# Optimization experiments

Hardware: AMD Instinct MI355X
Metric: run time of the kernel (lower is better)

## Reference

```python
import jax, jax.numpy as jnp
import numpy as np

N_NODES = 100000
N_EDGES = 1600000
DIM_IN, DIM_H, DIM_OUT = 128, 128, 64


def setup_inputs() -> dict:
    key = jax.random.key(0)
    ks = jax.random.split(key, 8)
    s = 0.05
    return {
        "x": jax.random.normal(ks[0], (N_NODES, DIM_IN), jnp.float32),
        "edge_index": jax.random.randint(ks[1], (2, N_EDGES), 0, N_NODES, jnp.int64),
        "W_l1": jax.random.normal(ks[2], (DIM_IN, DIM_H), jnp.float32) * s,
        "W_r1": jax.random.normal(ks[3], (DIM_IN, DIM_H), jnp.float32) * s,
        "b1": jax.random.normal(ks[4], (DIM_H,), jnp.float32) * s,
        "W_l2": jax.random.normal(ks[5], (DIM_H, DIM_OUT), jnp.float32) * s,
        "W_r2": jax.random.normal(ks[6], (DIM_H, DIM_OUT), jnp.float32) * s,
        "b2": jax.random.normal(ks[7], (DIM_OUT,), jnp.float32) * s,
    }


def _sage_conv(h, src, dst, n_nodes, W_l, W_r, b):
    # mean-aggregate neighbor features: gather x[src], scatter-sum to dst, divide by in-degree
    msg = h[src]                                              # [E, d]
    agg = jax.ops.segment_sum(msg, dst, num_segments=n_nodes)  # [N, d]
    deg = jax.ops.segment_sum(jnp.ones((src.shape[0],), h.dtype), dst, num_segments=n_nodes)
    mean = agg / jnp.maximum(deg, 1.0)[:, None]
    # out = lin_l(mean) + lin_r(x) ; bias lives on lin_l (PyG SAGEConv default)
    return mean @ W_l + h @ W_r + b


def reference(x, edge_index, W_l1, W_r1, b1, W_l2, W_r2, b2):
    src, dst = edge_index[0], edge_index[1]
    n = x.shape[0]
    h = jax.nn.relu(_sage_conv(x, src, dst, n, W_l1, W_r1, b1))
    # dropout(p=0.5) is identity in eval mode
    return _sage_conv(h, src, dst, n, W_l2, W_r2, b2)
```

## Files before the change

### kernel.cpp

```cpp
#include <hip/hip_runtime.h>

#define NN 100000
#define NE 1600000

typedef __attribute__((ext_vector_type(8))) short bf16x8;
typedef __attribute__((ext_vector_type(4))) float f32x4;

__device__ __forceinline__ float bf2f(unsigned short b) {
    union { unsigned int u; float f; } v;
    v.u = ((unsigned int)b) << 16;
    return v.f;
}
__device__ __forceinline__ unsigned short f2bf(float f) {
    union { float f; unsigned int u; } v; v.f = f;
    unsigned int u = v.u;
    return (unsigned short)((u + 0x7FFFu + ((u >> 16) & 1u)) >> 16);
}

__global__ void detect_kernel(const int* __restrict__ e, int* __restrict__ flag) {
    int t = blockIdx.x * blockDim.x + threadIdx.x;
    if (t < 4096 && e[2 * t + 1] != 0) atomicOr(flag, 1);
}

__device__ __forceinline__ int esrc(const int* e, int mode, int i) {
    return mode ? e[i] : e[2 * i];
}
__device__ __forceinline__ int edst(const int* e, int mode, int i) {
    return mode ? e[NE + i] : e[2 * (NE + i)];
}

__global__ __launch_bounds__(256) void wcvt_kernel(
    const float* __restrict__ W_l1, const float* __restrict__ W_r1,
    const float* __restrict__ W_l2, const float* __restrict__ W_r2,
    unsigned short* __restrict__ wt) {
    int b = blockIdx.x;
    const float* src; unsigned short* dst; int NO, tk, tn;
    if (b < 4)       { src = W_l1; dst = wt;         NO = 128; tk = b >> 1; tn = b & 1; }
    else if (b < 8)  { b -= 4; src = W_r1; dst = wt + 16384; NO = 128; tk = b >> 1; tn = b & 1; }
    else if (b < 10) { b -= 8; src = W_l2; dst = wt + 32768; NO = 64; tk = b; tn = 0; }
    else             { b -= 10; src = W_r2; dst = wt + 40960; NO = 64; tk = b; tn = 0; }
    __shared__ unsigned short lt[64][72];
    const int r0 = tk * 64, c0 = tn * 64;
    const int lr = threadIdx.x >> 6;
    const int lc = threadIdx.x & 63;
#pragma unroll
    for (int i = 0; i < 16; i++) {
        int r = lr * 16 + i;
        lt[lc][r] = f2bf(src[(size_t)(r0 + r) * NO + c0 + lc]);
    }
    __syncthreads();
#pragma unroll
    for (int i = 0; i < 16; i++) {
        int n = lr * 16 + i;
        dst[(size_t)(c0 + n) * 128 + r0 + lc] = lt[n][lc];
    }
}

#define NRANGE 4
#define RSZ 25000
#define NCHUNK 64
#define EPC (NE / NCHUNK)
#define GS 100352

__global__ __launch_bounds__(1024) void histA_kernel(
    const int* __restrict__ e, const int* __restrict__ flag, int* __restrict__ G) {
    __shared__ int lh[RSZ];
    const int bid = blockIdx.x;
    const int r = bid & (NRANGE - 1);
    const int c = bid >> 2;
    const int lo = r * RSZ;
    for (int idx = threadIdx.x; idx < RSZ; idx += 1024) lh[idx] = 0;
    __syncthreads();
    const int mode = *flag;
    const int base = c * EPC;
    for (int i = base + threadIdx.x; i < base + EPC; i += 1024) {
        int dl = edst(e, mode, i) - lo;
        if ((unsigned)dl < (unsigned)RSZ) atomicAdd(&lh[dl], 1);
    }
    __syncthreads();
    for (int idx = threadIdx.x; idx < RSZ; idx += 1024)
        G[(size_t)c * GS + lo + idx] = lh[idx];
}

__global__ __launch_bounds__(1024) void scatterC_kernel(
    const int* __restrict__ e, const int* __restrict__ flag,
    const int* __restrict__ S, const int* __restrict__ G, int* __restrict__ csr) {
    __shared__ int sOff[RSZ];
    const int bid = blockIdx.x;
    const int r = bid & (NRANGE - 1);
    const int c = bid >> 2;
    const int lo = r * RSZ;
    for (int idx = threadIdx.x; idx < RSZ; idx += 1024)
        sOff[idx] = S[lo + idx] + G[(size_t)c * GS + lo + idx];
    __syncthreads();
    const int mode = *flag;
    const int base = c * EPC;
    for (int i = base + threadIdx.x; i < base + EPC; i += 1024) {
        int dl = edst(e, mode, i) - lo;
        if ((unsigned)dl < (unsigned)RSZ) {
            int s = esrc(e, mode, i);
            csr[atomicAdd(&sOff[dl], 1)] = s;
        }
    }
}

#define PREF_B 391
#define CVT_G 6250

__global__ __launch_bounds__(256) void prefix_cvt_kernel(
    int* __restrict__ G, int* __restrict__ S,
    const float* __restrict__ xin, unsigned short* __restrict__ xb) {
    if (blockIdx.x < PREF_B) {
        int d = blockIdx.x * 256 + threadIdx.x;
        if (d >= NN) return;
        int run = 0;
#pragma unroll 8
        for (int c = 0; c < NCHUNK; c++) {
            size_t idx = (size_t)c * GS + d;
            int t = G[idx];
            G[idx] = run;
            run += t;
        }
        S[d] = run;
    } else {
        long long i = ((long long)(blockIdx.x - PREF_B) * 256 + threadIdx.x) * 8;
        float4 a = *(const float4*)(xin + i);
        float4 b = *(const float4*)(xin + i + 4);
        bf16x8 rv;
        rv[0] = (short)f2bf(a.x); rv[1] = (short)f2bf(a.y);
        rv[2] = (short)f2bf(a.z); rv[3] = (short)f2bf(a.w);
        rv[4] = (short)f2bf(b.x); rv[5] = (short)f2bf(b.y);
        rv[6] = (short)f2bf(b.z); rv[7] = (short)f2bf(b.w);
        *(bf16x8*)(xb + i) = rv;
    }
}

#define SCAN_G 392

__global__ __launch_bounds__(256) void blocksum_kernel(const int* __restrict__ S,
                                                       int* __restrict__ part) {
    int i = blockIdx.x * 256 + threadIdx.x;
    int v = (i < NN) ? S[i] : 0;
#pragma unroll
    for (int off = 32; off; off >>= 1) v += __shfl_down(v, off, 64);
    __shared__ int wsum[4];
    if ((threadIdx.x & 63) == 0) wsum[threadIdx.x >> 6] = v;
    __syncthreads();
    if (threadIdx.x == 0)
        part[blockIdx.x] = wsum[0] + wsum[1] + wsum[2] + wsum[3];
}

__global__ __launch_bounds__(512) void partscan_kernel(int* __restrict__ part) {
    __shared__ int lds[512];
    const int t = threadIdx.x;
    int v = (t < SCAN_G) ? part[t] : 0;
    lds[t] = v;
    __syncthreads();
    for (int off = 1; off < 512; off <<= 1) {
        int u = (t >= off) ? lds[t - off] : 0;
        __syncthreads();
        lds[t] += u;
        __syncthreads();
    }
    if (t < SCAN_G) part[t] = lds[t] - v;
}

__global__ __launch_bounds__(256) void scanfin_kernel(int* __restrict__ S,
                                                      const int* __restrict__ part) {
    __shared__ int lds[256];
    const int t = threadIdx.x;
    const int i = blockIdx.x * 256 + t;
    int v = (i < NN) ? S[i] : 0;
    lds[t] = v;
    __syncthreads();
    for (int off = 1; off < 256; off <<= 1) {
        int u = (t >= off) ? lds[t - off] : 0;
        __syncthreads();
        lds[t] += u;
        __syncthreads();
    }
    if (i < NN) S[i] = lds[t] - v + part[blockIdx.x];
}

__global__ __launch_bounds__(256) void gather_mean128(
    const unsigned short* __restrict__ feat, const int* __restrict__ csr,
    const int* __restrict__ S, unsigned short* __restrict__ out) {
    const int tid = threadIdx.x;
    const int node = blockIdx.x * 16 + (tid >> 4);
    const int c = tid & 15;
    if (node >= NN) return;
    const int begin = S[node];
    const int end = (node == NN - 1) ? NE : S[node + 1];
    float acc0[8] = {0.f, 0.f, 0.f, 0.f, 0.f, 0.f, 0.f, 0.f};
    float acc1[8] = {0.f, 0.f, 0.f, 0.f, 0.f, 0.f, 0.f, 0.f};
    int j = begin;
    for (; j + 4 <= end; j += 4) {
        int s0 = csr[j], s1 = csr[j + 1], s2 = csr[j + 2], s3 = csr[j + 3];
        bf16x8 v0 = *(const bf16x8*)(feat + (size_t)s0 * 128 + 8 * c);
        bf16x8 v1 = *(const bf16x8*)(feat + (size_t)s1 * 128 + 8 * c);
        bf16x8 v2 = *(const bf16x8*)(feat + (size_t)s2 * 128 + 8 * c);
        bf16x8 v3 = *(const bf16x8*)(feat + (size_t)s3 * 128 + 8 * c);
#pragma unroll
        for (int q = 0; q < 8; q++) {
            acc0[q] += bf2f((unsigned short)v0[q]) + bf2f((unsigned short)v2[q]);
            acc1[q] += bf2f((unsigned short)v1[q]) + bf2f((unsigned short)v3[q]);
        }
    }
    for (; j < end; j++) {
        int s = csr[j];
        bf16x8 v = *(const bf16x8*)(feat + (size_t)s * 128 + 8 * c);
#pragma unroll
        for (int q = 0; q < 8; q++) acc0[q] += bf2f((unsigned short)v[q]);
    }
    const float inv = 1.0f / fmaxf((float)(end - begin), 1.0f);
    bf16x8 r;
#pragma unroll
    for (int q = 0; q < 8; q++) r[q] = (short)f2bf((acc0[q] + acc1[q]) * inv);
    *(bf16x8*)(out + (size_t)node * 128 + 8 * c) = r;
}

__global__ __launch_bounds__(256) void gemm1_kernel(
    const unsigned short* __restrict__ A,
    const unsigned short* __restrict__ X,
    const unsigned short* __restrict__ WaT,
    const unsigned short* __restrict__ WbT,
    const float* __restrict__ b1,
    unsigned short* __restrict__ H, int N) {
    const int tid = threadIdx.x;
    const int lane = tid & 63;
    const int wv = tid >> 6;
    const int r16 = lane & 15;
    const int kg = lane >> 4;
    const long long rowbase = (long long)blockIdx.x * 128 + wv * 32;

    bf16x8 xf[2][4], af[2][4];
    const bf16x8 zz = {0, 0, 0, 0, 0, 0, 0, 0};
#pragma unroll
    for (int rt = 0; rt < 2; rt++) {
        long long row = rowbase + rt * 16 + r16;
        bool ok = row < N;
#pragma unroll
        for (int ks = 0; ks < 4; ks++) {
            xf[rt][ks] = ok ? *(const bf16x8*)(X + row * 128 + ks * 32 + kg * 8) : zz;
            af[rt][ks] = ok ? *(const bf16x8*)(A + row * 128 + ks * 32 + kg * 8) : zz;
        }
    }

    f32x4 acc[2][8];
#pragma unroll
    for (int t = 0; t < 8; t++) {
        float bv = b1[t * 16 + r16];
#pragma unroll
        for (int rt = 0; rt < 2; rt++) acc[rt][t] = (f32x4){bv, bv, bv, bv};
    }

#pragma unroll
    for (int t = 0; t < 8; t++) {
        const unsigned short* wb = WbT + (size_t)(t * 16 + r16) * 128 + kg * 8;
        const unsigned short* wa = WaT + (size_t)(t * 16 + r16) * 128 + kg * 8;
        bf16x8 bb[4], ba[4];
#pragma unroll
        for (int ks = 0; ks < 4; ks++) {
            bb[ks] = *(const bf16x8*)(wb + ks * 32);
            ba[ks] = *(const bf16x8*)(wa + ks * 32);
        }
#pragma unroll
        for (int rt = 0; rt < 2; rt++) {
#pragma unroll
            for (int ks = 0; ks < 4; ks++) {
                acc[rt][t] = __builtin_amdgcn_mfma_f32_16x16x32_bf16(
                    xf[rt][ks], bb[ks], acc[rt][t], 0, 0, 0);
                acc[rt][t] = __builtin_amdgcn_mfma_f32_16x16x32_bf16(
                    af[rt][ks], ba[ks], acc[rt][t], 0, 0, 0);
            }
        }
    }

#pragma unroll
    for (int rt = 0; rt < 2; rt++)
#pragma unroll
        for (int r = 0; r < 4; r++) {
            long long row = rowbase + rt * 16 + kg * 4 + r;
            if (row < N)
#pragma unroll
                for (int t = 0; t < 8; t++)
                    H[row * 128 + t * 16 + r16] = f2bf(fmaxf(acc[rt][t][r], 0.f));
        }
}

__global__ __launch_bounds__(256) void gemm23_kernel(
    const unsigned short* __restrict__ Hb,
    const unsigned short* __restrict__ WlT,
    const unsigned short* __restrict__ WrT,
    const float* __restrict__ b2,
    unsigned short* __restrict__ T2, unsigned short* __restrict__ P3, int N) {
    const int tid = threadIdx.x;
    const int lane = tid & 63;
    const int wv = tid >> 6;
    const int r16 = lane & 15;
    const int kg = lane >> 4;
    const long long rowbase = (long long)blockIdx.x * 128 + wv * 32;

    bf16x8 hf[2][4];
    const bf16x8 zz = {0, 0, 0, 0, 0, 0, 0, 0};
#pragma unroll
    for (int rt = 0; rt < 2; rt++) {
        long long row = rowbase + rt * 16 + r16;
        bool ok = row < N;
#pragma unroll
        for (int ks = 0; ks < 4; ks++)
            hf[rt][ks] = ok ? *(const bf16x8*)(Hb + row * 128 + ks * 32 + kg * 8) : zz;
    }

    f32x4 ot[2][4], op[2][4];
#pragma unroll
    for (int t = 0; t < 4; t++) {
        float bv = b2[t * 16 + r16];
#pragma unroll
        for (int rt = 0; rt < 2; rt++) {
            ot[rt][t] = (f32x4){0.f, 0.f, 0.f, 0.f};
            op[rt][t] = (f32x4){bv, bv, bv, bv};
        }
    }

#pragma unroll
    for (int t = 0; t < 4; t++) {
        const unsigned short* wl = WlT + (size_t)(t * 16 + r16) * 128 + kg * 8;
        const unsigned short* wr = WrT + (size_t)(t * 16 + r16) * 128 + kg * 8;
        bf16x8 bl[4], br[4];
#pragma unroll
        for (int ks = 0; ks < 4; ks++) {
            bl[ks] = *(const bf16x8*)(wl + ks * 32);
            br[ks] = *(const bf16x8*)(wr + ks * 32);
        }
#pragma unroll
        for (int rt = 0; rt < 2; rt++) {
#pragma unroll
            for (int ks = 0; ks < 4; ks++) {
                ot[rt][t] = __builtin_amdgcn_mfma_f32_16x16x32_bf16(
                    hf[rt][ks], bl[ks], ot[rt][t], 0, 0, 0);
                op[rt][t] = __builtin_amdgcn_mfma_f32_16x16x32_bf16(
                    hf[rt][ks], br[ks], op[rt][t], 0, 0, 0);
            }
        }
    }

#pragma unroll
    for (int rt = 0; rt < 2; rt++)
#pragma unroll
        for (int r = 0; r < 4; r++) {
            long long row = rowbase + rt * 16 + kg * 4 + r;
            if (row < N)
#pragma unroll
                for (int t = 0; t < 4; t++) {
                    T2[row * 64 + t * 16 + r16] = f2bf(ot[rt][t][r]);
                    P3[row * 64 + t * 16 + r16] = f2bf(op[rt][t][r]);
                }
        }
}

__global__ __launch_bounds__(256) void gather2_fused(
    const unsigned short* __restrict__ t2, const unsigned short* __restrict__ p3,
    const int* __restrict__ csr, const int* __restrict__ S, float* __restrict__ out) {
    const int tid = threadIdx.x;
    const int node = blockIdx.x * 32 + (tid >> 3);
    const int c = tid & 7;
    if (node >= NN) return;
    const int begin = S[node];
    const int end = (node == NN - 1) ? NE : S[node + 1];
    float acc0[8] = {0.f, 0.f, 0.f, 0.f, 0.f, 0.f, 0.f, 0.f};
    float acc1[8] = {0.f, 0.f, 0.f, 0.f, 0.f, 0.f, 0.f, 0.f};
    int j = begin;
    for (; j + 4 <= end; j += 4) {
        int s0 = csr[j], s1 = csr[j + 1], s2 = csr[j + 2], s3 = csr[j + 3];
        bf16x8 v0 = *(const bf16x8*)(t2 + (size_t)s0 * 64 + 8 * c);
        bf16x8 v1 = *(const bf16x8*)(t2 + (size_t)s1 * 64 + 8 * c);
        bf16x8 v2 = *(const bf16x8*)(t2 + (size_t)s2 * 64 + 8 * c);
        bf16x8 v3 = *(const bf16x8*)(t2 + (size_t)s3 * 64 + 8 * c);
#pragma unroll
        for (int q = 0; q < 8; q++) {
            acc0[q] += bf2f((unsigned short)v0[q]) + bf2f((unsigned short)v2[q]);
            acc1[q] += bf2f((unsigned short)v1[q]) + bf2f((unsigned short)v3[q]);
        }
    }
    for (; j < end; j++) {
        int s = csr[j];
        bf16x8 v = *(const bf16x8*)(t2 + (size_t)s * 64 + 8 * c);
#pragma unroll
        for (int q = 0; q < 8; q++) acc0[q] += bf2f((unsigned short)v[q]);
    }
    const float inv = 1.0f / fmaxf((float)(end - begin), 1.0f);
    bf16x8 pv = *(const bf16x8*)(p3 + (size_t)node * 64 + 8 * c);
    f32x4 r0, r1;
#pragma unroll
    for (int q = 0; q < 4; q++) {
        r0[q] = (acc0[q] + acc1[q]) * inv + bf2f((unsigned short)pv[q]);
        r1[q] = (acc0[4 + q] + acc1[4 + q]) * inv + bf2f((unsigned short)pv[4 + q]);
    }
    *(f32x4*)(out + (size_t)node * 64 + 8 * c) = r0;
    *(f32x4*)(out + (size_t)node * 64 + 8 * c + 4) = r1;
}

extern "C" void kernel_launch(void* const* d_in, const int* in_sizes, int n_in,
                              void* d_out, int out_size, void* d_ws, size_t ws_size,
                              hipStream_t stream) {
    const float* x    = (const float*)d_in[0];
    const int*   e32  = (const int*)d_in[1];
    const float* W_l1 = (const float*)d_in[2];
    const float* W_r1 = (const float*)d_in[3];
    const float* b1   = (const float*)d_in[4];
    const float* W_l2 = (const float*)d_in[5];
    const float* W_r2 = (const float*)d_in[6];
    const float* b2   = (const float*)d_in[7];
    float* out = (float*)d_out;

    int* wsI = (int*)d_ws;
    int* flag = wsI;
    int* S    = wsI + 1024;
    int* part = wsI + 101376;
    int* csr  = wsI + 101888;
    unsigned short* xb = (unsigned short*)(wsI + 1701888);
    unsigned short* t2b = (unsigned short*)(wsI + 1701888);
    unsigned short* p3b = (unsigned short*)(wsI + 4901888);
    int* G = wsI + 8101888;
    unsigned short* mean1b = (unsigned short*)(wsI + 8101888);
    unsigned short* hb     = (unsigned short*)(wsI + 14524416);
    unsigned short* wt     = (unsigned short*)(wsI + 20924416);

    hipMemsetAsync(d_ws, 0, 4096, stream);

    detect_kernel<<<16, 256, 0, stream>>>(e32, flag);
    wcvt_kernel<<<12, 256, 0, stream>>>(W_l1, W_r1, W_l2, W_r2, wt);
    histA_kernel<<<NRANGE * NCHUNK, 1024, 0, stream>>>(e32, flag, G);
    prefix_cvt_kernel<<<PREF_B + CVT_G, 256, 0, stream>>>(G, S, x, xb);
    blocksum_kernel<<<SCAN_G, 256, 0, stream>>>(S, part);
    partscan_kernel<<<1, 512, 0, stream>>>(part);
    scanfin_kernel<<<SCAN_G, 256, 0, stream>>>(S, part);
    scatterC_kernel<<<NRANGE * NCHUNK, 1024, 0, stream>>>(e32, flag, S, G, csr);

    gather_mean128<<<6250, 256, 0, stream>>>(xb, csr, S, mean1b);

    gemm1_kernel<<<782, 256, 0, stream>>>(mean1b, xb, wt, wt + 16384, b1, hb, NN);

    gemm23_kernel<<<782, 256, 0, stream>>>(hb, wt + 32768, wt + 40960, b2,
                                           t2b, p3b, NN);

    gather2_fused<<<3125, 256, 0, stream>>>(t2b, p3b, csr, S, out);
}
```

Before: 237.3 us.

## Store features column-blocked and split gathers into per-XCD column groups

The node feature buffers (x in bf16, mean1, h, t2) move from row-major to a column-group-major layout of 16-element groups. The gather kernels are split so each block handles one column group, chosen by blockIdx & 7 so it lines up with XCD round-robin scheduling. Each group's slice is then smaller and more likely to stay in one XCD's L2 during the random neighbor reads. Weight conversion to bf16 is folded into the GEMM kernels through LDS, which removes a launch but redoes the conversion in every block. The gathers also spread edges across lanes with shuffle reductions and use nontemporal loads and stores.

```diff
diff --git a/kernel.cpp b/kernel.cpp
--- a/kernel.cpp
+++ b/kernel.cpp
@@ -2,6 +2,7 @@
 
 #define NN 100000
 #define NE 1600000
+#define NN16 ((size_t)NN * 16)
 
 typedef __attribute__((ext_vector_type(8))) short bf16x8;
 typedef __attribute__((ext_vector_type(4))) float f32x4;
@@ -27,33 +28,6 @@
 }
 __device__ __forceinline__ int edst(const int* e, int mode, int i) {
     return mode ? e[NE + i] : e[2 * (NE + i)];
-}
-
-__global__ __launch_bounds__(256) void wcvt_kernel(
-    const float* __restrict__ W_l1, const float* __restrict__ W_r1,
-    const float* __restrict__ W_l2, const float* __restrict__ W_r2,
-    unsigned short* __restrict__ wt) {
-    int b = blockIdx.x;
-    const float* src; unsigned short* dst; int NO, tk, tn;
-    if (b < 4)       { src = W_l1; dst = wt;         NO = 128; tk = b >> 1; tn = b & 1; }
-    else if (b < 8)  { b -= 4; src = W_r1; dst = wt + 16384; NO = 128; tk = b >> 1; tn = b & 1; }
-    else if (b < 10) { b -= 8; src = W_l2; dst = wt + 32768; NO = 64; tk = b; tn = 0; }
-    else             { b -= 10; src = W_r2; dst = wt + 40960; NO = 64; tk = b; tn = 0; }
-    __shared__ unsigned short lt[64][72];
-    const int r0 = tk * 64, c0 = tn * 64;
-    const int lr = threadIdx.x >> 6;
-    const int lc = threadIdx.x & 63;
-#pragma unroll
-    for (int i = 0; i < 16; i++) {
-        int r = lr * 16 + i;
-        lt[lc][r] = f2bf(src[(size_t)(r0 + r) * NO + c0 + lc]);
-    }
-    __syncthreads();
-#pragma unroll
-    for (int i = 0; i < 16; i++) {
-        int n = lr * 16 + i;
-        dst[(size_t)(c0 + n) * 128 + r0 + lc] = lt[n][lc];
-    }
 }
 
 #define NRANGE 4
@@ -123,15 +97,19 @@
         }
         S[d] = run;
     } else {
-        long long i = ((long long)(blockIdx.x - PREF_B) * 256 + threadIdx.x) * 8;
-        float4 a = *(const float4*)(xin + i);
-        float4 b = *(const float4*)(xin + i + 4);
+        long long i = (long long)(blockIdx.x - PREF_B) * 256 + threadIdx.x;
+        int n = (int)(i >> 4);
+        int chunk = (int)(i & 15);
+        int g = chunk >> 1, off = (chunk & 1) * 8;
+        const float* src = xin + (size_t)n * 128 + chunk * 8;
+        float4 a = *(const float4*)(src);
+        float4 b = *(const float4*)(src + 4);
         bf16x8 rv;
         rv[0] = (short)f2bf(a.x); rv[1] = (short)f2bf(a.y);
         rv[2] = (short)f2bf(a.z); rv[3] = (short)f2bf(a.w);
         rv[4] = (short)f2bf(b.x); rv[5] = (short)f2bf(b.y);
         rv[6] = (short)f2bf(b.z); rv[7] = (short)f2bf(b.w);
-        *(bf16x8*)(xb + i) = rv;
+        *(bf16x8*)(xb + (size_t)g * NN16 + (size_t)n * 16 + off) = rv;
     }
 }
 
@@ -182,51 +160,75 @@
     if (i < NN) S[i] = lds[t] - v + part[blockIdx.x];
 }
 
-__global__ __launch_bounds__(256) void gather_mean128(
-    const unsigned short* __restrict__ feat, const int* __restrict__ csr,
-    const int* __restrict__ S, unsigned short* __restrict__ out) {
-    const int tid = threadIdx.x;
-    const int node = blockIdx.x * 16 + (tid >> 4);
-    const int c = tid & 15;
+__global__ __launch_bounds__(256) void gather128_col(
+    const unsigned short* __restrict__ xb, const int* __restrict__ csr,
+    const int* __restrict__ S, unsigned short* __restrict__ mean1) {
+    const int g = blockIdx.x & 7;
+    const int q = blockIdx.x >> 3;
+    const int lane8 = threadIdx.x & 7;
+    const int node = q * 32 + (threadIdx.x >> 3);
     if (node >= NN) return;
+    const int half = lane8 & 1;
+    const int slot = lane8 >> 1;
     const int begin = S[node];
     const int end = (node == NN - 1) ? NE : S[node + 1];
+    const unsigned short* base = xb + (size_t)g * NN16 + half * 8;
     float acc0[8] = {0.f, 0.f, 0.f, 0.f, 0.f, 0.f, 0.f, 0.f};
     float acc1[8] = {0.f, 0.f, 0.f, 0.f, 0.f, 0.f, 0.f, 0.f};
-    int j = begin;
-    for (; j + 4 <= end; j += 4) {
-        int s0 = csr[j], s1 = csr[j + 1], s2 = csr[j + 2], s3 = csr[j + 3];
-        bf16x8 v0 = *(const bf16x8*)(feat + (size_t)s0 * 128 + 8 * c);
-        bf16x8 v1 = *(const bf16x8*)(feat + (size_t)s1 * 128 + 8 * c);
-        bf16x8 v2 = *(const bf16x8*)(feat + (size_t)s2 * 128 + 8 * c);
-        bf16x8 v3 = *(const bf16x8*)(feat + (size_t)s3 * 128 + 8 * c);
-#pragma unroll
-        for (int q = 0; q < 8; q++) {
-            acc0[q] += bf2f((unsigned short)v0[q]) + bf2f((unsigned short)v2[q]);
-            acc1[q] += bf2f((unsigned short)v1[q]) + bf2f((unsigned short)v3[q]);
-        }
-    }
-    for (; j < end; j++) {
-        int s = csr[j];
-        bf16x8 v = *(const bf16x8*)(feat + (size_t)s * 128 + 8 * c);
-#pragma unroll
-        for (int q = 0; q < 8; q++) acc0[q] += bf2f((unsigned short)v[q]);
-    }
-    const float inv = 1.0f / fmaxf((float)(end - begin), 1.0f);
-    bf16x8 r;
-#pragma unroll
-    for (int q = 0; q < 8; q++) r[q] = (short)f2bf((acc0[q] + acc1[q]) * inv);
-    *(bf16x8*)(out + (size_t)node * 128 + 8 * c) = r;
-}
-
-__global__ __launch_bounds__(256) void gemm1_kernel(
+    int j = begin + slot;
+    for (; j + 4 < end; j += 8) {
+        int s0 = __builtin_nontemporal_load(csr + j);
+        int s1 = __builtin_nontemporal_load(csr + j + 4);
+        bf16x8 v0 = *(const bf16x8*)(base + (size_t)s0 * 16);
+        bf16x8 v1 = *(const bf16x8*)(base + (size_t)s1 * 16);
+#pragma unroll
+        for (int p = 0; p < 8; p++) {
+            acc0[p] += bf2f((unsigned short)v0[p]);
+            acc1[p] += bf2f((unsigned short)v1[p]);
+        }
+    }
+    if (j < end) {
+        int s = __builtin_nontemporal_load(csr + j);
+        bf16x8 v = *(const bf16x8*)(base + (size_t)s * 16);
+#pragma unroll
+        for (int p = 0; p < 8; p++) acc0[p] += bf2f((unsigned short)v[p]);
+    }
+#pragma unroll
+    for (int p = 0; p < 8; p++) {
+        float a = acc0[p] + acc1[p];
+        a += __shfl_xor(a, 2, 64);
+        a += __shfl_xor(a, 4, 64);
+        acc0[p] = a;
+    }
+    if (slot == 0) {
+        const float inv = 1.0f / fmaxf((float)(end - begin), 1.0f);
+        bf16x8 r;
+#pragma unroll
+        for (int p = 0; p < 8; p++) r[p] = (short)f2bf(acc0[p] * inv);
+        __builtin_nontemporal_store(
+            r, (bf16x8*)(mean1 + (size_t)g * NN16 + (size_t)node * 16 + half * 8));
+    }
+}
+
+__global__ __launch_bounds__(256, 2) void gemm1_kernel(
     const unsigned short* __restrict__ A,
     const unsigned short* __restrict__ X,
-    const unsigned short* __restrict__ WaT,
-    const unsigned short* __restrict__ WbT,
+    const float* __restrict__ Wa,
+    const float* __restrict__ Wb,
     const float* __restrict__ b1,
-    unsigned short* __restrict__ H, int N) {
+    unsigned short* __restrict__ H,
+    int N) {
+    constexpr int PITCH = 136;
+    __shared__ unsigned short sWa[128 * PITCH];
+    __shared__ unsigned short sWb[128 * PITCH];
     const int tid = threadIdx.x;
+    for (int idx = tid; idx < 128 * 128; idx += 256) {
+        int k = idx >> 7, n = idx & 127;
+        sWa[n * PITCH + k] = f2bf(Wa[idx]);
+        sWb[n * PITCH + k] = f2bf(Wb[idx]);
+    }
+    __syncthreads();
+
     const int lane = tid & 63;
     const int wv = tid >> 6;
     const int r16 = lane & 15;
@@ -241,8 +243,9 @@
         bool ok = row < N;
 #pragma unroll
         for (int ks = 0; ks < 4; ks++) {
-            xf[rt][ks] = ok ? *(const bf16x8*)(X + row * 128 + ks * 32 + kg * 8) : zz;
-            af[rt][ks] = ok ? *(const bf16x8*)(A + row * 128 + ks * 32 + kg * 8) : zz;
+            size_t off = (size_t)(2 * ks + (kg >> 1)) * NN16 + (size_t)row * 16 + (kg & 1) * 8;
+            xf[rt][ks] = ok ? *(const bf16x8*)(X + off) : zz;
+            af[rt][ks] = ok ? *(const bf16x8*)(A + off) : zz;
         }
     }
 
@@ -256,13 +259,13 @@
 
 #pragma unroll
     for (int t = 0; t < 8; t++) {
-        const unsigned short* wb = WbT + (size_t)(t * 16 + r16) * 128 + kg * 8;
-        const unsigned short* wa = WaT + (size_t)(t * 16 + r16) * 128 + kg * 8;
+        const unsigned short* wp = &sWb[(t * 16 + r16) * PITCH + kg * 8];
+        const unsigned short* wq = &sWa[(t * 16 + r16) * PITCH + kg * 8];
         bf16x8 bb[4], ba[4];
 #pragma unroll
         for (int ks = 0; ks < 4; ks++) {
-            bb[ks] = *(const bf16x8*)(wb + ks * 32);
-            ba[ks] = *(const bf16x8*)(wa + ks * 32);
+            bb[ks] = *(const bf16x8*)(wp + ks * 32);
+            ba[ks] = *(const bf16x8*)(wq + ks * 32);
         }
 #pragma unroll
         for (int rt = 0; rt < 2; rt++) {
@@ -284,17 +287,30 @@
             if (row < N)
 #pragma unroll
                 for (int t = 0; t < 8; t++)
-                    H[row * 128 + t * 16 + r16] = f2bf(fmaxf(acc[rt][t][r], 0.f));
+                    H[(size_t)t * NN16 + (size_t)row * 16 + r16] =
+                        f2bf(fmaxf(acc[rt][t][r], 0.f));
         }
 }
 
 __global__ __launch_bounds__(256) void gemm23_kernel(
     const unsigned short* __restrict__ Hb,
-    const unsigned short* __restrict__ WlT,
-    const unsigned short* __restrict__ WrT,
+    const float* __restrict__ Wl,
+    const float* __restrict__ Wr,
     const float* __restrict__ b2,
-    unsigned short* __restrict__ T2, unsigned short* __restrict__ P3, int N) {
+    unsigned short* __restrict__ T2,
+    unsigned short* __restrict__ P3,
+    int N) {
+    constexpr int PITCH = 136;
+    __shared__ unsigned short sWl[64 * PITCH];
+    __shared__ unsigned short sWr[64 * PITCH];
     const int tid = threadIdx.x;
+    for (int idx = tid; idx < 128 * 64; idx += 256) {
+        int k = idx >> 6, n = idx & 63;
+        sWl[n * PITCH + k] = f2bf(Wl[idx]);
+        sWr[n * PITCH + k] = f2bf(Wr[idx]);
+    }
+    __syncthreads();
+
     const int lane = tid & 63;
     const int wv = tid >> 6;
     const int r16 = lane & 15;
@@ -308,8 +324,10 @@
         long long row = rowbase + rt * 16 + r16;
         bool ok = row < N;
 #pragma unroll
-        for (int ks = 0; ks < 4; ks++)
-            hf[rt][ks] = ok ? *(const bf16x8*)(Hb + row * 128 + ks * 32 + kg * 8) : zz;
+        for (int ks = 0; ks < 4; ks++) {
+            size_t off = (size_t)(2 * ks + (kg >> 1)) * NN16 + (size_t)row * 16 + (kg & 1) * 8;
+            hf[rt][ks] = ok ? *(const bf16x8*)(Hb + off) : zz;
+        }
     }
 
     f32x4 ot[2][4], op[2][4];
@@ -325,8 +343,8 @@
 
 #pragma unroll
     for (int t = 0; t < 4; t++) {
-        const unsigned short* wl = WlT + (size_t)(t * 16 + r16) * 128 + kg * 8;
-        const unsigned short* wr = WrT + (size_t)(t * 16 + r16) * 128 + kg * 8;
+        const unsigned short* wl = &sWl[(t * 16 + r16) * PITCH + kg * 8];
+        const unsigned short* wr = &sWr[(t * 16 + r16) * PITCH + kg * 8];
         bf16x8 bl[4], br[4];
 #pragma unroll
         for (int ks = 0; ks < 4; ks++) {
@@ -353,52 +371,68 @@
             if (row < N)
 #pragma unroll
                 for (int t = 0; t < 4; t++) {
-                    T2[row * 64 + t * 16 + r16] = f2bf(ot[rt][t][r]);
-                    P3[row * 64 + t * 16 + r16] = f2bf(op[rt][t][r]);
+                    T2[(size_t)t * NN16 + (size_t)row * 16 + r16] = f2bf(ot[rt][t][r]);
+                    P3[(size_t)row * 64 + t * 16 + r16] = f2bf(op[rt][t][r]);
                 }
         }
 }
 
-__global__ __launch_bounds__(256) void gather2_fused(
+__global__ __launch_bounds__(256) void gather2_col(
     const unsigned short* __restrict__ t2, const unsigned short* __restrict__ p3,
     const int* __restrict__ csr, const int* __restrict__ S, float* __restrict__ out) {
-    const int tid = threadIdx.x;
-    const int node = blockIdx.x * 32 + (tid >> 3);
-    const int c = tid & 7;
-    if (node >= NN) return;
+    const int xcd = blockIdx.x & 7;
+    const int g2 = xcd >> 1;
+    const int nh = xcd & 1;
+    const int q = blockIdx.x >> 3;
+    const int lane8 = threadIdx.x & 7;
+    const int node = nh * (NN / 2) + q * 32 + (threadIdx.x >> 3);
+    if (node >= nh * (NN / 2) + (NN / 2)) return;
+    const int half = lane8 & 1;
+    const int slot = lane8 >> 1;
     const int begin = S[node];
     const int end = (node == NN - 1) ? NE : S[node + 1];
+    const unsigned short* base = t2 + (size_t)g2 * NN16 + half * 8;
     float acc0[8] = {0.f, 0.f, 0.f, 0.f, 0.f, 0.f, 0.f, 0.f};
     float acc1[8] = {0.f, 0.f, 0.f, 0.f, 0.f, 0.f, 0.f, 0.f};
-    int j = begin;
-    for (; j + 4 <= end; j += 4) {
-        int s0 = csr[j], s1 = csr[j + 1], s2 = csr[j + 2], s3 = csr[j + 3];
-        bf16x8 v0 = *(const bf16x8*)(t2 + (size_t)s0 * 64 + 8 * c);
-        bf16x8 v1 = *(const bf16x8*)(t2 + (size_t)s1 * 64 + 8 * c);
-        bf16x8 v2 = *(const bf16x8*)(t2 + (size_t)s2 * 64 + 8 * c);
-        bf16x8 v3 = *(const bf16x8*)(t2 + (size_t)s3 * 64 + 8 * c);
-#pragma unroll
-        for (int q = 0; q < 8; q++) {
-            acc0[q] += bf2f((unsigned short)v0[q]) + bf2f((unsigned short)v2[q]);
-            acc1[q] += bf2f((unsigned short)v1[q]) + bf2f((unsigned short)v3[q]);
-        }
-    }
-    for (; j < end; j++) {
-        int s = csr[j];
-        bf16x8 v = *(const bf16x8*)(t2 + (size_t)s * 64 + 8 * c);
-#pragma unroll
-        for (int q = 0; q < 8; q++) acc0[q] += bf2f((unsigned short)v[q]);
-    }
-    const float inv = 1.0f / fmaxf((float)(end - begin), 1.0f);
-    bf16x8 pv = *(const bf16x8*)(p3 + (size_t)node * 64 + 8 * c);
-    f32x4 r0, r1;
-#pragma unroll
-    for (int q = 0; q < 4; q++) {
-        r0[q] = (acc0[q] + acc1[q]) * inv + bf2f((unsigned short)pv[q]);
-        r1[q] = (acc0[4 + q] + acc1[4 + q]) * inv + bf2f((unsigned short)pv[4 + q]);
-    }
-    *(f32x4*)(out + (size_t)node * 64 + 8 * c) = r0;
-    *(f32x4*)(out + (size_t)node * 64 + 8 * c + 4) = r1;
+    int j = begin + slot;
+    for (; j + 4 < end; j += 8) {
+        int s0 = __builtin_nontemporal_load(csr + j);
+        int s1 = __builtin_nontemporal_load(csr + j + 4);
+        bf16x8 v0 = *(const bf16x8*)(base + (size_t)s0 * 16);
+        bf16x8 v1 = *(const bf16x8*)(base + (size_t)s1 * 16);
+#pragma unroll
+        for (int p = 0; p < 8; p++) {
+            acc0[p] += bf2f((unsigned short)v0[p]);
+            acc1[p] += bf2f((unsigned short)v1[p]);
+        }
+    }
+    if (j < end) {
+        int s = __builtin_nontemporal_load(csr + j);
+        bf16x8 v = *(const bf16x8*)(base + (size_t)s * 16);
+#pragma unroll
+        for (int p = 0; p < 8; p++) acc0[p] += bf2f((unsigned short)v[p]);
+    }
+#pragma unroll
+    for (int p = 0; p < 8; p++) {
+        float a = acc0[p] + acc1[p];
+        a += __shfl_xor(a, 2, 64);
+        a += __shfl_xor(a, 4, 64);
+        acc0[p] = a;
+    }
+    if (slot == 0) {
+        const float inv = 1.0f / fmaxf((float)(end - begin), 1.0f);
+        const bf16x8 pv = __builtin_nontemporal_load(
+            (const bf16x8*)(p3 + (size_t)node * 64 + g2 * 16 + half * 8));
+        f32x4 r0, r1;
+#pragma unroll
+        for (int p = 0; p < 4; p++) {
+            r0[p] = acc0[p] * inv + bf2f((unsigned short)pv[p]);
+            r1[p] = acc0[4 + p] * inv + bf2f((unsigned short)pv[4 + p]);
+        }
+        float* o = out + (size_t)node * 64 + g2 * 16 + half * 8;
+        __builtin_nontemporal_store(r0, (f32x4*)o);
+        __builtin_nontemporal_store(r1, (f32x4*)(o + 4));
+    }
 }
 
 extern "C" void kernel_launch(void* const* d_in, const int* in_sizes, int n_in,
@@ -419,18 +453,16 @@
     int* S    = wsI + 1024;
     int* part = wsI + 101376;
     int* csr  = wsI + 101888;
-    unsigned short* xb = (unsigned short*)(wsI + 1701888);
+    unsigned short* xb  = (unsigned short*)(wsI + 1701888);
     unsigned short* t2b = (unsigned short*)(wsI + 1701888);
     unsigned short* p3b = (unsigned short*)(wsI + 4901888);
     int* G = wsI + 8101888;
     unsigned short* mean1b = (unsigned short*)(wsI + 8101888);
     unsigned short* hb     = (unsigned short*)(wsI + 14524416);
-    unsigned short* wt     = (unsigned short*)(wsI + 20924416);
 
     hipMemsetAsync(d_ws, 0, 4096, stream);
 
     detect_kernel<<<16, 256, 0, stream>>>(e32, flag);
-    wcvt_kernel<<<12, 256, 0, stream>>>(W_l1, W_r1, W_l2, W_r2, wt);
     histA_kernel<<<NRANGE * NCHUNK, 1024, 0, stream>>>(e32, flag, G);
     prefix_cvt_kernel<<<PREF_B + CVT_G, 256, 0, stream>>>(G, S, x, xb);
     blocksum_kernel<<<SCAN_G, 256, 0, stream>>>(S, part);
@@ -438,12 +470,11 @@
     scanfin_kernel<<<SCAN_G, 256, 0, stream>>>(S, part);
     scatterC_kernel<<<NRANGE * NCHUNK, 1024, 0, stream>>>(e32, flag, S, G, csr);
 
-    gather_mean128<<<6250, 256, 0, stream>>>(xb, csr, S, mean1b);
-
-    gemm1_kernel<<<782, 256, 0, stream>>>(mean1b, xb, wt, wt + 16384, b1, hb, NN);
-
-    gemm23_kernel<<<782, 256, 0, stream>>>(hb, wt + 32768, wt + 40960, b2,
-                                           t2b, p3b, NN);
-
-    gather2_fused<<<3125, 256, 0, stream>>>(t2b, p3b, csr, S, out);
-}
+    gather128_col<<<3125 * 8, 256, 0, stream>>>(xb, csr, S, mean1b);
+
+    gemm1_kernel<<<782, 256, 0, stream>>>(mean1b, xb, W_l1, W_r1, b1, hb, NN);
+
+    gemm23_kernel<<<782, 256, 0, stream>>>(hb, W_l2, W_r2, b2, t2b, p3b, NN);
+
+    gather2_col<<<1563 * 8, 256, 0, stream>>>(t2b, p3b, csr, S, out);
+}
```

New measurement: 301.0 us. 26.8% more time.
